# Kernel tuning notes

Hardware: AMD Instinct MI355X
Metric: run time of the kernel (lower is better)

The kernel has to match this reference:

```python
import jax, jax.numpy as jnp
import numpy as np

PAD = 16      # ReplicationPad2d(16)
KW = 33       # per-block kernel is 33x33
PATCH = 36    # 36x36 input patch per 4x4 output block
BLK = 4       # output block size


def setup_inputs() -> dict:
    key = jax.random.key(0)
    k1, k2 = jax.random.split(key)
    inputImg = jax.random.normal(k1, (1, 3, 512, 512), dtype=jnp.float32)
    Kernels = jax.random.uniform(k2, (1, KW * KW, 512 // BLK, 512 // BLK), dtype=jnp.float32)
    return {"inputImg": inputImg, "Kernels": Kernels}


def reference(inputImg, Kernels):
    B, C, H, W = inputImg.shape
    HB, WB = H // BLK, W // BLK
    # replication pad == edge pad
    padded = jnp.pad(inputImg, ((0, 0), (0, 0), (PAD, PAD), (PAD, PAD)), mode="edge")
    # gather overlapping 36x36 patches, one per 4x4 block (stride 4)
    idx_h = BLK * jnp.arange(HB)[:, None] + jnp.arange(PATCH)[None, :]  # [HB,36]
    idx_w = BLK * jnp.arange(WB)[:, None] + jnp.arange(PATCH)[None, :]  # [WB,36]
    tmp = padded[:, :, idx_h, :]            # [B,C,HB,36,Wp]
    patches = tmp[:, :, :, :, idx_w]        # [B,C,HB,36,WB,36]
    # per-block 33x33 kernel: Kernels[0, u*33+v, h, w] -> K[u,v,h,w]
    K = Kernels[0].reshape(KW, KW, HB, WB)
    # valid conv: out offset (oi,oj) in the 4x4 block
    rows = []
    for oi in range(BLK):
        cols = []
        for oj in range(BLK):
            win = patches[:, :, :, oi:oi + KW, :, oj:oj + KW]  # [B,C,HB,33,WB,33]
            cols.append(jnp.einsum("bchuwv,uvhw->bchw", win, K))
        rows.append(jnp.stack(cols, axis=-1))   # [B,C,HB,WB,4]
    out = jnp.stack(rows, axis=-2)              # [B,C,HB,WB,4,4]
    out = out.transpose(0, 1, 2, 4, 3, 5).reshape(B, C, H, W)
    return out
```

## Files before the change

### kernel.cpp

```cpp
#include <hip/hip_runtime.h>

#define HH 512
#define WW 512
#define PD 544
#define PADN (3 * PD * PD)
#define OUTN (3 * HH * WW)
#define NB 128
#define KSTR 16384

__global__ __launch_bounds__(256) void pad_kernel(const float* __restrict__ img,
                                                  unsigned short* __restrict__ gpad,
                                                  float* __restrict__ out) {
    int idx = blockIdx.x * 256 + threadIdx.x;
    if (idx < OUTN) out[idx] = 0.0f;
    if (idx >= PADN) return;
    int c  = idx / (PD * PD);
    int r  = idx - c * (PD * PD);
    int py = r / PD;
    int px = r - py * PD;
    int iy = min(max(py - 16, 0), HH - 1);
    int ix = min(max(px - 16, 0), WW - 1);
    union { float f; unsigned u; } v;
    v.f = img[(c * HH + iy) * WW + ix];
    unsigned u = v.u + 0x7FFFu + ((v.u >> 16) & 1u);
    gpad[idx] = (unsigned short)(u >> 16);
}

__device__ __forceinline__ void async16u(const unsigned short* g, unsigned short* l) {
    __builtin_amdgcn_global_load_lds((const __attribute__((address_space(1))) void*)g,
                                     (__attribute__((address_space(3))) void*)l, 16, 0, 0);
}
__device__ __forceinline__ float bflo(unsigned d) { union { unsigned u; float f; } x; x.u = d << 16;         return x.f; }
__device__ __forceinline__ float bfhi(unsigned d) { union { unsigned u; float f; } x; x.u = d & 0xFFFF0000u; return x.f; }

__global__ __launch_bounds__(256, 2) void reblur_kernel(const unsigned short* __restrict__ gpad,
                                                        const float* __restrict__ Kern,
                                                        float* __restrict__ out) {
    __shared__ unsigned short s_img[8][3][288];

    const int lane = threadIdx.x & 63;
    const int dy   = threadIdx.x >> 6;
    const int uq   = blockIdx.x >> 8;
    const int bb   = blockIdx.x & 255;
    const int h    = bb >> 1;
    const int wt   = bb & 1;
    const int ua   = uq ? (8 * uq + 1) : 0;
    const int n    = uq ? 8 : 9;
    const int kofs = h * NB + wt * 64 + lane;

    if (lane < 36) {
        const int r = 4 * h + ua + dy;
#pragma unroll
        for (int c = 0; c < 3; ++c)
            async16u(gpad + ((size_t)(c * PD + r) * PD + 256 * wt) + 8 * lane,
                     &s_img[r & 7][c][0]);
    }

    float acc[3][4];
#pragma unroll
    for (int c = 0; c < 3; ++c)
#pragma unroll
        for (int oj = 0; oj < 4; ++oj) acc[c][oj] = 0.0f;

#pragma unroll 1
    for (int t = 0; t < n; ++t) {
        asm volatile("s_waitcnt vmcnt(0)" ::: "memory");
        __builtin_amdgcn_s_barrier();

        float wA[33];
#pragma unroll
        for (int v = 0; v < 33; ++v)
            wA[v] = Kern[(size_t)((ua + t) * 33 + v) * KSTR + kofs];

        if (t + 1 < n && dy == (t & 3) && lane < 36) {
            const int r = 4 * h + ua + t + 4;
#pragma unroll
            for (int c = 0; c < 3; ++c)
                async16u(gpad + ((size_t)(c * PD + r) * PD + 256 * wt) + 8 * lane,
                         &s_img[r & 7][c][0]);
        }

        const int slot = (4 * h + ua + t + dy) & 7;
#pragma unroll
        for (int c = 0; c < 3; ++c) {
            float wf[36];
            const unsigned short* sp = &s_img[slot][c][4 * lane];
#pragma unroll
            for (int j = 0; j < 9; ++j) {
                const uint2 dd = *(const uint2*)(sp + 4 * j);
                wf[4 * j + 0] = bflo(dd.x);
                wf[4 * j + 1] = bfhi(dd.x);
                wf[4 * j + 2] = bflo(dd.y);
                wf[4 * j + 3] = bfhi(dd.y);
            }
#pragma unroll
            for (int v = 0; v < 33; ++v) {
#pragma unroll
                for (int oj = 0; oj < 4; ++oj)
                    acc[c][oj] = fmaf(wf[v + oj], wA[v], acc[c][oj]);
            }
        }
    }

    const int xb = 4 * (wt * 64 + lane);
#pragma unroll
    for (int c = 0; c < 3; ++c) {
        float* op = out + (size_t)(c * HH + 4 * h + dy) * WW + xb;
#pragma unroll
        for (int oj = 0; oj < 4; ++oj) atomicAdd(op + oj, acc[c][oj]);
    }
}

__global__ __launch_bounds__(256) void reblur_naive(const float* __restrict__ img,
                                                    const float* __restrict__ Kern,
                                                    float* __restrict__ out) {
    const int lane = threadIdx.x & 63;
    const int dy   = threadIdx.x >> 6;
    const int c    = blockIdx.x >> 8;
    const int bb   = blockIdx.x & 255;
    const int h    = bb >> 1;
    const int wt   = bb & 1;
    const int wb   = wt * 64 + lane;
    const int y    = 4 * h + dy;

    float acc[4] = {0.f, 0.f, 0.f, 0.f};
    const float* kb = Kern + h * NB + wb;
#pragma unroll 1
    for (int u = 0; u < 33; ++u) {
        const int iy = min(max(y + u - 16, 0), HH - 1);
        float row[36];
#pragma unroll
        for (int e = 0; e < 36; ++e) {
            const int ix = min(max(4 * wb + e - 16, 0), WW - 1);
            row[e]       = img[(c * HH + iy) * WW + ix];
        }
#pragma unroll
        for (int v = 0; v < 33; ++v) {
            const float w = kb[(u * 33 + v) * KSTR];
#pragma unroll
            for (int oj = 0; oj < 4; ++oj)
                acc[oj] = fmaf(row[v + oj], w, acc[oj]);
        }
    }
    float4 o;
    o.x = acc[0]; o.y = acc[1]; o.z = acc[2]; o.w = acc[3];
    *reinterpret_cast<float4*>(out + (size_t)(c * HH + y) * WW + 4 * wb) = o;
}

extern "C" void kernel_launch(void* const* d_in, const int* in_sizes, int n_in,
                              void* d_out, int out_size, void* d_ws, size_t ws_size,
                              hipStream_t stream) {
    const float* img  = (const float*)d_in[0];
    const float* Kern = (const float*)d_in[1];
    float* out        = (float*)d_out;

    if (ws_size >= (size_t)PADN * sizeof(unsigned short)) {
        unsigned short* gpad = (unsigned short*)d_ws;
        pad_kernel<<<(PADN + 255) / 256, 256, 0, stream>>>(img, gpad, out);
        reblur_kernel<<<1024, 256, 0, stream>>>(gpad, Kern, out);
    } else {
        reblur_naive<<<768, 256, 0, stream>>>(img, Kern, out);
    }
}
```

Measured before the change: 149.5 us.

## Replace bf16 LDS-staged reblur with direct fp32 global-load kernel using packed FMA

The padded image is now stored as fp32 instead of bf16, and the main kernel drops the LDS ring buffer and its barriers. Each thread reads its image rows straight from global memory, and the grid is reorganised into 256 blocks of 1024 threads, each handling 16 output rows, both width halves and a 4-or-5 row slice of u. Accumulation uses 2-wide float vectors so the compiler can emit packed FMA. This removes the bf16 convert cost and the per-step barriers, and improves accuracy. In exchange it doubles the image bytes read and relies on cache for reuse. It also launches fewer, larger blocks and issues more atomics into each output, since u is split into 8 slices instead of 4.

```diff
diff --git a/kernel.cpp b/kernel.cpp
--- a/kernel.cpp
+++ b/kernel.cpp
@@ -8,9 +8,11 @@
 #define NB 128
 #define KSTR 16384
 
-__global__ __launch_bounds__(256) void pad_kernel(const float* __restrict__ img,
-                                                  unsigned short* __restrict__ gpad,
-                                                  float* __restrict__ out) {
+typedef float f2 __attribute__((ext_vector_type(2)));
+
+__global__ __launch_bounds__(256) void pad_f32(const float* __restrict__ img,
+                                               float* __restrict__ gpad,
+                                               float* __restrict__ out) {
     int idx = blockIdx.x * 256 + threadIdx.x;
     if (idx < OUTN) out[idx] = 0.0f;
     if (idx >= PADN) return;
@@ -20,94 +22,77 @@
     int px = r - py * PD;
     int iy = min(max(py - 16, 0), HH - 1);
     int ix = min(max(px - 16, 0), WW - 1);
-    union { float f; unsigned u; } v;
-    v.f = img[(c * HH + iy) * WW + ix];
-    unsigned u = v.u + 0x7FFFu + ((v.u >> 16) & 1u);
-    gpad[idx] = (unsigned short)(u >> 16);
+    gpad[idx] = img[(c * HH + iy) * WW + ix];
 }
 
-__device__ __forceinline__ void async16u(const unsigned short* g, unsigned short* l) {
-    __builtin_amdgcn_global_load_lds((const __attribute__((address_space(1))) void*)g,
-                                     (__attribute__((address_space(3))) void*)l, 16, 0, 0);
-}
-__device__ __forceinline__ float bflo(unsigned d) { union { unsigned u; float f; } x; x.u = d << 16;         return x.f; }
-__device__ __forceinline__ float bfhi(unsigned d) { union { unsigned u; float f; } x; x.u = d & 0xFFFF0000u; return x.f; }
+__global__ __launch_bounds__(1024, 2) void reblur_direct(const float* __restrict__ gpad,
+                                                         const float* __restrict__ Kern,
+                                                         float* __restrict__ out) {
+    const int tid  = threadIdx.x;
+    const int lane = tid & 63;
+    const int w16  = tid >> 6;
+    const int b    = blockIdx.x;
+    const int uq   = b >> 5;
+    const int hq   = b & 31;
+    const int orow = 16 * hq + w16;
+    const int h    = orow >> 2;
+    const int u0   = uq ? (4 * uq + 1) : 0;
+    const int nu   = uq ? 4 : 5;
 
-__global__ __launch_bounds__(256, 2) void reblur_kernel(const unsigned short* __restrict__ gpad,
-                                                        const float* __restrict__ Kern,
-                                                        float* __restrict__ out) {
-    __shared__ unsigned short s_img[8][3][288];
-
-    const int lane = threadIdx.x & 63;
-    const int dy   = threadIdx.x >> 6;
-    const int uq   = blockIdx.x >> 8;
-    const int bb   = blockIdx.x & 255;
-    const int h    = bb >> 1;
-    const int wt   = bb & 1;
-    const int ua   = uq ? (8 * uq + 1) : 0;
-    const int n    = uq ? 8 : 9;
-    const int kofs = h * NB + wt * 64 + lane;
-
-    if (lane < 36) {
-        const int r = 4 * h + ua + dy;
-#pragma unroll
-        for (int c = 0; c < 3; ++c)
-            async16u(gpad + ((size_t)(c * PD + r) * PD + 256 * wt) + 8 * lane,
-                     &s_img[r & 7][c][0]);
-    }
-
-    float acc[3][4];
+    f2 aL[3][2], aH[3][2];
 #pragma unroll
     for (int c = 0; c < 3; ++c)
 #pragma unroll
-        for (int oj = 0; oj < 4; ++oj) acc[c][oj] = 0.0f;
+        for (int hf = 0; hf < 2; ++hf) { aL[c][hf] = (f2)(0.0f); aH[c][hf] = (f2)(0.0f); }
 
 #pragma unroll 1
-    for (int t = 0; t < n; ++t) {
-        asm volatile("s_waitcnt vmcnt(0)" ::: "memory");
-        __builtin_amdgcn_s_barrier();
-
-        float wA[33];
+    for (int t = 0; t < nu; ++t) {
+        const int u = u0 + t;
+        const size_t krow = (size_t)(u * 33) * KSTR + (size_t)h * NB;
 #pragma unroll
-        for (int v = 0; v < 33; ++v)
-            wA[v] = Kern[(size_t)((ua + t) * 33 + v) * KSTR + kofs];
-
-        if (t + 1 < n && dy == (t & 3) && lane < 36) {
-            const int r = 4 * h + ua + t + 4;
+        for (int hf = 0; hf < 2; ++hf) {
+            const int w = hf * 64 + lane;
+            float wv[33];
 #pragma unroll
-            for (int c = 0; c < 3; ++c)
-                async16u(gpad + ((size_t)(c * PD + r) * PD + 256 * wt) + 8 * lane,
-                         &s_img[r & 7][c][0]);
-        }
-
-        const int slot = (4 * h + ua + t + dy) & 7;
+            for (int v = 0; v < 33; ++v)
+                wv[v] = Kern[krow + (size_t)v * KSTR + w];
 #pragma unroll
-        for (int c = 0; c < 3; ++c) {
-            float wf[36];
-            const unsigned short* sp = &s_img[slot][c][4 * lane];
+            for (int c = 0; c < 3; ++c) {
+                const float* ip = gpad + ((size_t)c * PD + orow + u) * PD + 4 * w;
+                float wf[36];
 #pragma unroll
-            for (int j = 0; j < 9; ++j) {
-                const uint2 dd = *(const uint2*)(sp + 4 * j);
-                wf[4 * j + 0] = bflo(dd.x);
-                wf[4 * j + 1] = bfhi(dd.x);
-                wf[4 * j + 2] = bflo(dd.y);
-                wf[4 * j + 3] = bfhi(dd.y);
-            }
+                for (int j = 0; j < 9; ++j) {
+                    const float4 rr = *(const float4*)(ip + 4 * j);
+                    wf[4 * j + 0] = rr.x;
+                    wf[4 * j + 1] = rr.y;
+                    wf[4 * j + 2] = rr.z;
+                    wf[4 * j + 3] = rr.w;
+                }
+                f2 l = aL[c][hf], hh = aH[c][hf];
 #pragma unroll
-            for (int v = 0; v < 33; ++v) {
-#pragma unroll
-                for (int oj = 0; oj < 4; ++oj)
-                    acc[c][oj] = fmaf(wf[v + oj], wA[v], acc[c][oj]);
+                for (int v = 0; v < 33; ++v) {
+                    const f2 w2 = {wv[v], wv[v]};
+                    const f2 xl = {wf[v + 0], wf[v + 1]};
+                    const f2 xh = {wf[v + 2], wf[v + 3]};
+                    l  = xl * w2 + l;
+                    hh = xh * w2 + hh;
+                }
+                aL[c][hf] = l; aH[c][hf] = hh;
             }
         }
     }
 
-    const int xb = 4 * (wt * 64 + lane);
 #pragma unroll
     for (int c = 0; c < 3; ++c) {
-        float* op = out + (size_t)(c * HH + 4 * h + dy) * WW + xb;
+        float* orow_p = out + ((size_t)c * HH + orow) * WW;
 #pragma unroll
-        for (int oj = 0; oj < 4; ++oj) atomicAdd(op + oj, acc[c][oj]);
+        for (int hf = 0; hf < 2; ++hf) {
+            float* op = orow_p + 4 * (hf * 64 + lane);
+            atomicAdd(op + 0, aL[c][hf].x);
+            atomicAdd(op + 1, aL[c][hf].y);
+            atomicAdd(op + 2, aH[c][hf].x);
+            atomicAdd(op + 3, aH[c][hf].y);
+        }
     }
 }
 
@@ -154,10 +139,10 @@
     const float* Kern = (const float*)d_in[1];
     float* out        = (float*)d_out;
 
-    if (ws_size >= (size_t)PADN * sizeof(unsigned short)) {
-        unsigned short* gpad = (unsigned short*)d_ws;
-        pad_kernel<<<(PADN + 255) / 256, 256, 0, stream>>>(img, gpad, out);
-        reblur_kernel<<<1024, 256, 0, stream>>>(gpad, Kern, out);
+    if (ws_size >= (size_t)PADN * sizeof(float)) {
+        float* gpad = (float*)d_ws;
+        pad_f32<<<(PADN + 255) / 256, 256, 0, stream>>>(img, gpad, out);
+        reblur_direct<<<256, 1024, 0, stream>>>(gpad, Kern, out);
     } else {
         reblur_naive<<<768, 256, 0, stream>>>(img, Kern, out);
     }
```

After: 254.3 us. +70.1%, slower.
